# Kernel tuning notes

Measured on AMD Instinct MI355X. Metric: run time of the kernel, lower is better.

## Reference

```python
import jax, jax.numpy as jnp
import numpy as np


def _phi(z, conv_w, conv_b):
    # z: (H, W, S, 1) -> 3x3 SAME conv over state channels -> softmax over states
    x = jnp.transpose(z[..., 0], (2, 0, 1))[None]  # (1, S, H, W)
    y = jax.lax.conv_general_dilated(
        x, conv_w, window_strides=(1, 1), padding='SAME',
        dimension_numbers=('NCHW', 'OIHW', 'NCHW')) + conv_b[None, :, None, None]
    return jax.nn.softmax(jnp.transpose(y[0], (1, 2, 0)), axis=2)[..., None]  # (H, W, S, 1)


def _update(obs, P, u_k, w_k_O, conv_w, conv_b):
    H, W, O = obs.shape
    S = P.shape[0]
    # b = P^T @ obs per cell: b[h,w,s] = sum_o P[o,s] * obs[h,w,o]
    b = jnp.einsum('os,hwo->hws', P, obs)[..., None]  # (H, W, S, 1)
    # Analytic Jacobian db/dP: deriv_b[h,w,s,0,i,j] = obs[h,w,i] * delta(s==j)
    eye = jnp.eye(S, O, dtype=obs.dtype)
    deriv_b = (obs[:, :, None, :, None] * eye[None, None, :, None, :])[:, :, :, None, :, :]  # (H,W,S,1,S,O)

    Bu = b * u_k                                  # (H, W, S, 1)
    bu = jnp.sum(Bu, axis=2, keepdims=True)       # (H, W, 1, 1)
    Z = Bu / bu                                   # Bu / bu

    u_kp1 = _phi(Z, conv_w, conv_b)               # (H, W, S, 1)

    # Sensitivity recursion for obs params (quotient rule on Bu/bu)
    du = deriv_b * u_k[..., None, None] + b[..., None, None] * w_k_O  # (H,W,S,1,S,O)
    term1 = du * bu[..., None, None]
    term2 = jnp.expand_dims(jnp.sum(du, axis=2), 3) * Bu[..., None, None]
    w_pre = (term1 - term2) / bu[..., None, None] ** 2                # (H,W,S,1,S,O)

    # J @ w  ==  9 JVPs of Phi at Z with tangent columns of w (exact, avoids dense (HWS)^2 Jacobian)
    tangents = jnp.moveaxis(w_pre.reshape(H, W, S, 1, S * O), -1, 0)  # (S*O, H, W, S, 1)
    jvp1 = lambda t: jax.jvp(lambda z: _phi(z, conv_w, conv_b), (Z,), (t,))[1]
    w_kp1_O = jnp.moveaxis(jax.vmap(jvp1)(tangents), 0, -1).reshape(H, W, S, 1, S, O)
    return u_kp1, w_kp1_O


def setup_inputs() -> dict:
    key = jax.random.key(0)
    k1, k2, k3 = jax.random.split(key, 3)
    H = W = 512
    S = O = 3
    obs = jax.random.uniform(k1, (H, W, O), dtype=jnp.float32)
    obs_param_matrix = jnp.ones((S, O), jnp.float32) / O          # row-stochastic init
    u_k = jnp.ones((H, W, S, 1), jnp.float32) / S                 # uniform belief
    w_k_O = jnp.zeros((H, W, S, 1, S, O), jnp.float32)
    conv_w = jax.random.normal(k2, (S, S, 3, 3), jnp.float32) * 0.1
    conv_b = jax.random.normal(k3, (S,), jnp.float32) * 0.1
    return {'obs': obs, 'obs_param_matrix': obs_param_matrix, 'u_k': u_k,
            'w_k_O': w_k_O, 'conv_w': conv_w, 'conv_b': conv_b}


def reference(obs, obs_param_matrix, u_k, w_k_O, conv_w, conv_b):
    return _update(obs, obs_param_matrix, u_k, w_k_O, conv_w, conv_b)
```

## Files before the change

kernel.cpp:

```cpp
#include <hip/hip_runtime.h>

#define IMH 512
#define IMW 512
#define TW 32
#define TH 8
#define HW_ (TW + 2)
#define HH_ (TH + 2)
#define NHALO (HW_ * HH_)
#define ROW 31

__global__ __launch_bounds__(256, 2)
void hmm_fused(const float* __restrict__ obs,
               const float* __restrict__ P,
               const float* __restrict__ u_k,
               const float* __restrict__ w_k,
               const float* __restrict__ conv_w,
               const float* __restrict__ conv_b,
               float* __restrict__ out) {
    __shared__ float lds[NHALO * ROW];

    const int tid = threadIdx.x;
    const int w0 = blockIdx.x * TW;
    const int h0 = blockIdx.y * TH;

    float Pm[9];
#pragma unroll
    for (int i = 0; i < 9; ++i) Pm[i] = P[i];

    for (int p = tid; p < NHALO; p += 256) {
        const int hh = h0 + p / HW_ - 1;
        const int ww = w0 + p % HW_ - 1;
        float* row = &lds[p * ROW];
        if (hh < 0 || hh >= IMH || ww < 0 || ww >= IMW) {
#pragma unroll
            for (int c = 0; c < 30; ++c) row[c] = 0.0f;
            continue;
        }
        const int pix = hh * IMW + ww;
        const float ov[3] = {obs[pix * 3 + 0], obs[pix * 3 + 1], obs[pix * 3 + 2]};
        const float us[3] = {u_k[pix * 3 + 0], u_k[pix * 3 + 1], u_k[pix * 3 + 2]};

        float b[3], Bu[3], bu = 0.0f;
#pragma unroll
        for (int s = 0; s < 3; ++s) {
            b[s] = Pm[0 * 3 + s] * ov[0] + Pm[1 * 3 + s] * ov[1] + Pm[2 * 3 + s] * ov[2];
            Bu[s] = b[s] * us[s];
            bu += Bu[s];
        }
        const float inv_bu = 1.0f / bu;
        float Z[3];
#pragma unroll
        for (int s = 0; s < 3; ++s) { Z[s] = Bu[s] * inv_bu; row[s] = Z[s]; }

        const float* wkp = &w_k[(size_t)pix * 27];
#pragma unroll
        for (int i = 0; i < 3; ++i) {
#pragma unroll
            for (int j = 0; j < 3; ++j) {
                const int ij = i * 3 + j;
                float du[3], sdu = 0.0f;
#pragma unroll
                for (int s = 0; s < 3; ++s) {
                    float d = b[s] * wkp[s * 9 + ij];
                    if (s == j) d += ov[i] * us[s];
                    du[s] = d;
                    sdu += d;
                }
#pragma unroll
                for (int s = 0; s < 3; ++s)
                    row[(1 + ij) * 3 + s] = (du[s] - sdu * Z[s]) * inv_bu;
            }
        }
    }

    float cw[81];
#pragma unroll
    for (int i = 0; i < 81; ++i) cw[i] = conv_w[i];
    const float cb[3] = {conv_b[0], conv_b[1], conv_b[2]};

    __syncthreads();

    const int tx = tid % TW, ty = tid / TW;
    const int hp = (ty + 1) * HW_ + (tx + 1);
    const int pix = (h0 + ty) * IMW + (w0 + tx);

    float p0, p1, p2;
    {
        float y[3] = {cb[0], cb[1], cb[2]};
#pragma unroll
        for (int ky = 0; ky < 3; ++ky) {
#pragma unroll
            for (int kx = 0; kx < 3; ++kx) {
                const float* nb = &lds[(hp + (ky - 1) * HW_ + (kx - 1)) * ROW];
                const float v0 = nb[0], v1 = nb[1], v2 = nb[2];
#pragma unroll
                for (int s = 0; s < 3; ++s)
                    y[s] += cw[s * 27 + 0 * 9 + ky * 3 + kx] * v0 +
                            cw[s * 27 + 1 * 9 + ky * 3 + kx] * v1 +
                            cw[s * 27 + 2 * 9 + ky * 3 + kx] * v2;
            }
        }
        const float m = fmaxf(y[0], fmaxf(y[1], y[2]));
        const float e0 = __expf(y[0] - m), e1 = __expf(y[1] - m), e2 = __expf(y[2] - m);
        const float inv = 1.0f / (e0 + e1 + e2);
        p0 = e0 * inv; p1 = e1 * inv; p2 = e2 * inv;
        out[pix * 3 + 0] = p0; out[pix * 3 + 1] = p1; out[pix * 3 + 2] = p2;
    }

    float wout[27];
#pragma unroll
    for (int g = 1; g < 10; ++g) {
        float a[3] = {0.0f, 0.0f, 0.0f};
#pragma unroll
        for (int ky = 0; ky < 3; ++ky) {
#pragma unroll
            for (int kx = 0; kx < 3; ++kx) {
                const float* nb = &lds[(hp + (ky - 1) * HW_ + (kx - 1)) * ROW];
                const float v0 = nb[g * 3 + 0], v1 = nb[g * 3 + 1], v2 = nb[g * 3 + 2];
#pragma unroll
                for (int s = 0; s < 3; ++s)
                    a[s] += cw[s * 27 + 0 * 9 + ky * 3 + kx] * v0 +
                            cw[s * 27 + 1 * 9 + ky * 3 + kx] * v1 +
                            cw[s * 27 + 2 * 9 + ky * 3 + kx] * v2;
            }
        }
        const float dot = p0 * a[0] + p1 * a[1] + p2 * a[2];
        const int ij = g - 1;
        wout[0 * 9 + ij] = p0 * (a[0] - dot);
        wout[1 * 9 + ij] = p1 * (a[1] - dot);
        wout[2 * 9 + ij] = p2 * (a[2] - dot);
    }

    __syncthreads();

#pragma unroll
    for (int c = 0; c < 27; ++c) lds[tid * 27 + c] = wout[c];
    __syncthreads();

    float* outw = out + IMH * IMW * 3;
    for (int idx = tid; idx < TW * TH * 27; idx += 256) {
        const int r = idx / (TW * 27);
        const int rem = idx - r * (TW * 27);
        outw[(h0 + r) * (IMW * 27) + w0 * 27 + rem] = lds[idx];
    }
}

extern "C" void kernel_launch(void* const* d_in, const int* in_sizes, int n_in,
                              void* d_out, int out_size, void* d_ws, size_t ws_size,
                              hipStream_t stream) {
    const float* obs    = (const float*)d_in[0];
    const float* P      = (const float*)d_in[1];
    const float* u_k    = (const float*)d_in[2];
    const float* w_k    = (const float*)d_in[3];
    const float* conv_w = (const float*)d_in[4];
    const float* conv_b = (const float*)d_in[5];
    float* out = (float*)d_out;

    dim3 grid(IMW / TW, IMH / TH);
    hmm_fused<<<grid, 256, 0, stream>>>(obs, P, u_k, w_k, conv_w, conv_b, out);
}
```

Before: 111.5 us.

## Pad LDS rows to 36 floats and use float4 loads in single fused stencil pass

The per-pixel halo row in shared memory is padded from 31 to 36 floats so it can be written and read as 16-byte float4 vectors. The convolution now visits each of the 9 neighbours once, accumulates all 10 channel groups (Z and the 9 tangents) together, and then applies the softmax and its JVP. Before, the LDS was read separately for every group with scalar loads. Occupancy hint is raised to 3 blocks per CU. The padding enlarges LDS per block (340*36*4 bytes, about 49 KB) and the 30 accumulators raise register pressure, which may conflict with the higher occupancy target.

```diff
diff --git a/kernel.cpp b/kernel.cpp
--- a/kernel.cpp
+++ b/kernel.cpp
@@ -7,9 +7,11 @@
 #define HW_ (TW + 2)
 #define HH_ (TH + 2)
 #define NHALO (HW_ * HH_)
-#define ROW 31
+#define ROWQ 9
 
-__global__ __launch_bounds__(256, 2)
+typedef float f4 __attribute__((ext_vector_type(4)));
+
+__global__ __launch_bounds__(256, 3)
 void hmm_fused(const float* __restrict__ obs,
                const float* __restrict__ P,
                const float* __restrict__ u_k,
@@ -17,7 +19,8 @@
                const float* __restrict__ conv_w,
                const float* __restrict__ conv_b,
                float* __restrict__ out) {
-    __shared__ float lds[NHALO * ROW];
+    __shared__ f4 lds4[NHALO * ROWQ];
+    float* lds = (float*)lds4;
 
     const int tid = threadIdx.x;
     const int w0 = blockIdx.x * TW;
@@ -30,105 +33,112 @@
     for (int p = tid; p < NHALO; p += 256) {
         const int hh = h0 + p / HW_ - 1;
         const int ww = w0 + p % HW_ - 1;
-        float* row = &lds[p * ROW];
+        f4* row4 = &lds4[p * ROWQ];
+        float va[32];
         if (hh < 0 || hh >= IMH || ww < 0 || ww >= IMW) {
 #pragma unroll
-            for (int c = 0; c < 30; ++c) row[c] = 0.0f;
-            continue;
+            for (int c = 0; c < 32; ++c) va[c] = 0.0f;
+        } else {
+            const int pix = hh * IMW + ww;
+            const float ov[3] = {obs[pix * 3 + 0], obs[pix * 3 + 1], obs[pix * 3 + 2]};
+            const float us[3] = {u_k[pix * 3 + 0], u_k[pix * 3 + 1], u_k[pix * 3 + 2]};
+
+            float b[3], Bu[3], bu = 0.0f;
+#pragma unroll
+            for (int s = 0; s < 3; ++s) {
+                b[s] = Pm[0 * 3 + s] * ov[0] + Pm[1 * 3 + s] * ov[1] + Pm[2 * 3 + s] * ov[2];
+                Bu[s] = b[s] * us[s];
+                bu += Bu[s];
+            }
+            const float inv_bu = 1.0f / bu;
+            float Z[3];
+#pragma unroll
+            for (int s = 0; s < 3; ++s) { Z[s] = Bu[s] * inv_bu; va[s] = Z[s]; }
+
+            const float* wkp = &w_k[(size_t)pix * 27];
+#pragma unroll
+            for (int i = 0; i < 3; ++i) {
+#pragma unroll
+                for (int j = 0; j < 3; ++j) {
+                    const int ij = i * 3 + j;
+                    float du[3], sdu = 0.0f;
+#pragma unroll
+                    for (int s = 0; s < 3; ++s) {
+                        float d = b[s] * wkp[s * 9 + ij];
+                        if (s == j) d += ov[i] * us[s];
+                        du[s] = d;
+                        sdu += d;
+                    }
+#pragma unroll
+                    for (int s = 0; s < 3; ++s)
+                        va[(1 + ij) * 3 + s] = (du[s] - sdu * Z[s]) * inv_bu;
+                }
+            }
+            va[30] = 0.0f; va[31] = 0.0f;
         }
-        const int pix = hh * IMW + ww;
-        const float ov[3] = {obs[pix * 3 + 0], obs[pix * 3 + 1], obs[pix * 3 + 2]};
-        const float us[3] = {u_k[pix * 3 + 0], u_k[pix * 3 + 1], u_k[pix * 3 + 2]};
-
-        float b[3], Bu[3], bu = 0.0f;
 #pragma unroll
-        for (int s = 0; s < 3; ++s) {
-            b[s] = Pm[0 * 3 + s] * ov[0] + Pm[1 * 3 + s] * ov[1] + Pm[2 * 3 + s] * ov[2];
-            Bu[s] = b[s] * us[s];
-            bu += Bu[s];
-        }
-        const float inv_bu = 1.0f / bu;
-        float Z[3];
-#pragma unroll
-        for (int s = 0; s < 3; ++s) { Z[s] = Bu[s] * inv_bu; row[s] = Z[s]; }
-
-        const float* wkp = &w_k[(size_t)pix * 27];
-#pragma unroll
-        for (int i = 0; i < 3; ++i) {
-#pragma unroll
-            for (int j = 0; j < 3; ++j) {
-                const int ij = i * 3 + j;
-                float du[3], sdu = 0.0f;
-#pragma unroll
-                for (int s = 0; s < 3; ++s) {
-                    float d = b[s] * wkp[s * 9 + ij];
-                    if (s == j) d += ov[i] * us[s];
-                    du[s] = d;
-                    sdu += d;
-                }
-#pragma unroll
-                for (int s = 0; s < 3; ++s)
-                    row[(1 + ij) * 3 + s] = (du[s] - sdu * Z[s]) * inv_bu;
-            }
-        }
+        for (int t = 0; t < 8; ++t)
+            row4[t] = (f4){va[4 * t + 0], va[4 * t + 1], va[4 * t + 2], va[4 * t + 3]};
     }
 
     float cw[81];
 #pragma unroll
     for (int i = 0; i < 81; ++i) cw[i] = conv_w[i];
-    const float cb[3] = {conv_b[0], conv_b[1], conv_b[2]};
+    const float cb0 = conv_b[0], cb1 = conv_b[1], cb2 = conv_b[2];
 
     __syncthreads();
 
-    const int tx = tid % TW, ty = tid / TW;
+    const int tx = tid & 31, ty = tid >> 5;
     const int hp = (ty + 1) * HW_ + (tx + 1);
     const int pix = (h0 + ty) * IMW + (w0 + tx);
 
-    float p0, p1, p2;
-    {
-        float y[3] = {cb[0], cb[1], cb[2]};
+    float acc[10][3];
 #pragma unroll
-        for (int ky = 0; ky < 3; ++ky) {
+    for (int g = 0; g < 10; ++g) { acc[g][0] = 0.0f; acc[g][1] = 0.0f; acc[g][2] = 0.0f; }
+    acc[0][0] = cb0; acc[0][1] = cb1; acc[0][2] = cb2;
+
 #pragma unroll
-            for (int kx = 0; kx < 3; ++kx) {
-                const float* nb = &lds[(hp + (ky - 1) * HW_ + (kx - 1)) * ROW];
-                const float v0 = nb[0], v1 = nb[1], v2 = nb[2];
+    for (int ky = 0; ky < 3; ++ky) {
+#pragma unroll
+        for (int kx = 0; kx < 3; ++kx) {
+            const f4* nb4 = &lds4[(hp + (ky - 1) * HW_ + (kx - 1)) * ROWQ];
+            const f4 q0 = nb4[0], q1 = nb4[1], q2 = nb4[2], q3 = nb4[3];
+            const f4 q4 = nb4[4], q5 = nb4[5], q6 = nb4[6], q7 = nb4[7];
+            float v[30];
+            v[0] = q0.x;  v[1] = q0.y;  v[2] = q0.z;  v[3] = q0.w;
+            v[4] = q1.x;  v[5] = q1.y;  v[6] = q1.z;  v[7] = q1.w;
+            v[8] = q2.x;  v[9] = q2.y;  v[10] = q2.z; v[11] = q2.w;
+            v[12] = q3.x; v[13] = q3.y; v[14] = q3.z; v[15] = q3.w;
+            v[16] = q4.x; v[17] = q4.y; v[18] = q4.z; v[19] = q4.w;
+            v[20] = q5.x; v[21] = q5.y; v[22] = q5.z; v[23] = q5.w;
+            v[24] = q6.x; v[25] = q6.y; v[26] = q6.z; v[27] = q6.w;
+            v[28] = q7.x; v[29] = q7.y;
+            const int t_ = ky * 3 + kx;
+#pragma unroll
+            for (int g = 0; g < 10; ++g) {
 #pragma unroll
                 for (int s = 0; s < 3; ++s)
-                    y[s] += cw[s * 27 + 0 * 9 + ky * 3 + kx] * v0 +
-                            cw[s * 27 + 1 * 9 + ky * 3 + kx] * v1 +
-                            cw[s * 27 + 2 * 9 + ky * 3 + kx] * v2;
+                    acc[g][s] += cw[s * 27 + 0 + t_] * v[g * 3 + 0] +
+                                 cw[s * 27 + 9 + t_] * v[g * 3 + 1] +
+                                 cw[s * 27 + 18 + t_] * v[g * 3 + 2];
             }
         }
-        const float m = fmaxf(y[0], fmaxf(y[1], y[2]));
-        const float e0 = __expf(y[0] - m), e1 = __expf(y[1] - m), e2 = __expf(y[2] - m);
-        const float inv = 1.0f / (e0 + e1 + e2);
-        p0 = e0 * inv; p1 = e1 * inv; p2 = e2 * inv;
-        out[pix * 3 + 0] = p0; out[pix * 3 + 1] = p1; out[pix * 3 + 2] = p2;
     }
+
+    const float m = fmaxf(acc[0][0], fmaxf(acc[0][1], acc[0][2]));
+    const float e0 = __expf(acc[0][0] - m), e1 = __expf(acc[0][1] - m), e2 = __expf(acc[0][2] - m);
+    const float inv = 1.0f / (e0 + e1 + e2);
+    const float p0 = e0 * inv, p1 = e1 * inv, p2 = e2 * inv;
+    out[pix * 3 + 0] = p0; out[pix * 3 + 1] = p1; out[pix * 3 + 2] = p2;
 
     float wout[27];
 #pragma unroll
     for (int g = 1; g < 10; ++g) {
-        float a[3] = {0.0f, 0.0f, 0.0f};
-#pragma unroll
-        for (int ky = 0; ky < 3; ++ky) {
-#pragma unroll
-            for (int kx = 0; kx < 3; ++kx) {
-                const float* nb = &lds[(hp + (ky - 1) * HW_ + (kx - 1)) * ROW];
-                const float v0 = nb[g * 3 + 0], v1 = nb[g * 3 + 1], v2 = nb[g * 3 + 2];
-#pragma unroll
-                for (int s = 0; s < 3; ++s)
-                    a[s] += cw[s * 27 + 0 * 9 + ky * 3 + kx] * v0 +
-                            cw[s * 27 + 1 * 9 + ky * 3 + kx] * v1 +
-                            cw[s * 27 + 2 * 9 + ky * 3 + kx] * v2;
-            }
-        }
-        const float dot = p0 * a[0] + p1 * a[1] + p2 * a[2];
+        const float dot = p0 * acc[g][0] + p1 * acc[g][1] + p2 * acc[g][2];
         const int ij = g - 1;
-        wout[0 * 9 + ij] = p0 * (a[0] - dot);
-        wout[1 * 9 + ij] = p1 * (a[1] - dot);
-        wout[2 * 9 + ij] = p2 * (a[2] - dot);
+        wout[0 * 9 + ij] = p0 * (acc[g][0] - dot);
+        wout[1 * 9 + ij] = p1 * (acc[g][1] - dot);
+        wout[2 * 9 + ij] = p2 * (acc[g][2] - dot);
     }
 
     __syncthreads();
```

After: 138.3 us. +24.0%, slower.
